# Performance work log

Hardware: AMD Instinct MI355X
Metric: run time of the kernel (lower is better)

The kernel has to match this reference:

```python
import jax, jax.numpy as jnp
import numpy as np

RCUT, RCUT_SMTH = 6.0, 0.5
NEURON = [25, 50, 100]
ATTN, NLAYER, AXIS, TEBD, NTYPES = 128, 2, 16, 8, 4
NF, NLOC, NNEI = 1, 4096, 120
LN_EPS = 1e-5


def setup_inputs() -> dict:
    key = jax.random.key(0)
    ks = jax.random.split(key, 24)
    rij = jax.random.normal(ks[0], (NF, NLOC, NNEI, 3), jnp.float32) * 2.0
    nmask = jax.random.uniform(ks[1], (NF, NLOC, NNEI)) < 0.9
    atype = jax.random.randint(ks[2], (NF, NLOC), 0, NTYPES, dtype=jnp.int32)
    ntype = jax.random.randint(ks[3], (NF, NLOC, NNEI), 0, NTYPES, dtype=jnp.int32)
    tebd = jax.random.normal(ks[4], (NTYPES, TEBD), jnp.float32) * 0.1
    dims = [1 + 2 * TEBD] + NEURON
    s = 0.1
    M = NEURON[-1]
    inp = dict(rij=rij, nmask=nmask, atype=atype, ntype=ntype, tebd=tebd)
    for i in range(3):
        inp[f'emb_w{i}'] = jax.random.normal(ks[5 + i], (dims[i], dims[i + 1]), jnp.float32) * s
        inp[f'emb_b{i}'] = jax.random.normal(ks[8 + i], (dims[i + 1],), jnp.float32) * s
    inp['wq'] = jax.random.normal(ks[11], (NLAYER, M, ATTN), jnp.float32) * s
    inp['bq'] = jax.random.normal(ks[12], (NLAYER, ATTN), jnp.float32) * s
    inp['wk'] = jax.random.normal(ks[13], (NLAYER, M, ATTN), jnp.float32) * s
    inp['bk'] = jax.random.normal(ks[14], (NLAYER, ATTN), jnp.float32) * s
    inp['wv'] = jax.random.normal(ks[15], (NLAYER, M, ATTN), jnp.float32) * s
    inp['bv'] = jax.random.normal(ks[16], (NLAYER, ATTN), jnp.float32) * s
    inp['wo'] = jax.random.normal(ks[17], (NLAYER, ATTN, M), jnp.float32) * s
    inp['bo'] = jax.random.normal(ks[18], (NLAYER, M), jnp.float32) * s
    inp['ln_g'] = jnp.ones((NLAYER, M), jnp.float32)
    inp['ln_b'] = jnp.zeros((NLAYER, M), jnp.float32)
    return inp


def _l2norm(t):
    return t / jnp.maximum(jnp.linalg.norm(t, axis=-1, keepdims=True), 1e-12)


def reference(rij, nmask, atype, ntype, tebd, emb_w0, emb_b0, emb_w1, emb_b1,
              emb_w2, emb_b2, wq, bq, wk, bk, wv, bv, wo, bo, ln_g, ln_b):
    f32 = jnp.float32
    m = nmask.astype(f32)                       # [F,N,K]
    r = jnp.linalg.norm(rij, axis=-1)           # neighbor distances
    # smooth switch function: 1 for r<rcut_smth, poly taper to 0 at rcut
    uu = jnp.clip((r - RCUT_SMTH) / (RCUT - RCUT_SMTH), 0.0, 1.0)
    sw = uu ** 3 * (-6.0 * uu ** 2 + 15.0 * uu - 10.0) + 1.0
    sr = sw / r * m                              # s(r), masked
    rhat = rij / r[..., None]                    # normalized rel. coords
    env = jnp.concatenate([sr[..., None], sr[..., None] * rhat], axis=-1)  # R^i [F,N,K,4]
    # embedding net input: s(r) ++ neighbor tebd ++ center tebd  (concat, two-side)
    t_nei = tebd[ntype]                                        # [F,N,K,TEBD]
    t_cen = jnp.broadcast_to(tebd[atype][:, :, None, :], t_nei.shape)
    x = jnp.concatenate([sr[..., None], t_nei, t_cen], axis=-1)
    h = jnp.tanh(x @ emb_w0 + emb_b0)
    h = jnp.tanh(h @ emb_w1 + emb_b1) + jnp.concatenate([h, h], -1)  # resnet (out=2*in)
    g = jnp.tanh(h @ emb_w2 + emb_b2) + jnp.concatenate([h, h], -1)  # G [F,N,K,M]
    g = g * m[..., None]
    # angular gate R_hat R_hat^T and pairwise mask / smooth weights
    gate = jnp.einsum('fnqc,fnkc->fnqk', rhat, rhat)
    sw_m = sw * m
    amask = nmask[..., :, None] & nmask[..., None, :]
    temp = float(np.sqrt(ATTN * 1.0))            # (attn*scaling_factor)**0.5
    neg = jnp.finfo(f32).min
    for l in range(NLAYER):
        q = _l2norm(g @ wq[l] + bq[l])
        k = _l2norm(g @ wk[l] + bk[l])
        v = _l2norm(g @ wv[l] + bv[l])
        scores = jnp.einsum('fnqd,fnkd->fnqk', q, k) / temp
        attnw = jax.nn.softmax(jnp.where(amask, scores, neg), axis=-1)
        attnw = attnw * amask.astype(f32)
        attnw = attnw * sw_m[..., :, None] * sw_m[..., None, :]   # smooth
        attnw = attnw * gate                                      # attn_dotr
        o = jnp.einsum('fnqk,fnkd->fnqd', attnw, v) @ wo[l] + bo[l]
        mu = o.mean(-1, keepdims=True)
        var = o.var(-1, keepdims=True)
        o = (o - mu) * jax.lax.rsqrt(var + LN_EPS) * ln_g[l] + ln_b[l]
        g = g + o                                # residual LayerNorm update
    g = g * m[..., None]
    gr = jnp.einsum('fnkc,fnkm->fncm', env, g) / NNEI            # [F,N,4,M]
    d = jnp.einsum('fncm,fnca->fnma', gr, gr[..., :AXIS])        # [F,N,M,AXIS]
    d = d.reshape(d.shape[0], d.shape[1], -1)
    return jnp.concatenate([d, tebd[atype]], axis=-1)            # concat_output_tebd
```

## Files before the change

### kernel.cpp

```cpp
#include <hip/hip_runtime.h>


#define NNEI 120
#define MDIM 100
#define ADIM 128
#define BP   136
#define H2P  72
#define XP   40
#define OUTD 1608

typedef __attribute__((ext_vector_type(8))) short bf16x8;
typedef __attribute__((ext_vector_type(4))) float f32x4;

__device__ __forceinline__ float bf2f(unsigned short u){
    return __uint_as_float(((unsigned int)u) << 16);
}
__device__ __forceinline__ unsigned short f2bf(float f){
    unsigned int x = __float_as_uint(f);
    return (unsigned short)((x + 0x7fffu + ((x >> 16) & 1u)) >> 16);
}
__device__ __forceinline__ unsigned int cvtpk(float lo, float hi){
    unsigned int r;
    asm("v_cvt_pk_bf16_f32 %0, %1, %2" : "=v"(r) : "v"(lo), "v"(hi));
    return r;
}
__device__ __forceinline__ float ftanh(float x){
    return 1.0f - 2.0f / (__expf(2.0f * x) + 1.0f);
}
__device__ __forceinline__ float red16(float v){
    v += __shfl_xor(v, 1, 64); v += __shfl_xor(v, 2, 64);
    v += __shfl_xor(v, 4, 64); v += __shfl_xor(v, 8, 64);
    return v;
}

__global__ void detect_mask_kernel(const unsigned char* __restrict__ p,
                                   int* __restrict__ flag){
    if (blockIdx.x == 0 && threadIdx.x == 0){
        const unsigned int* u = (const unsigned int*)p;
        int alli = 1, allf = 1;
        for (int i = 0; i < 64; ++i){
            unsigned int w = u[i];
            if (!(w == 0u || w == 1u)) alli = 0;
            if (!(w == 0u || w == 0x3f800000u)) allf = 0;
        }
        flag[0] = alli ? 1 : (allf ? 2 : 0);
    }
}

__global__ void prep_weights(const float* __restrict__ wq, const float* __restrict__ wk,
                             const float* __restrict__ wv, const float* __restrict__ wo,
                             const float* __restrict__ ew2, const float* __restrict__ ew0,
                             const float* __restrict__ ew1,
                             unsigned short* __restrict__ wsb){
    const int fid = blockIdx.x;
    const int lane = threadIdx.x;
    unsigned short* dst = wsb + (size_t)fid * 512 + lane * 8;
    if (fid < 192){
        const int l = fid / 96, rem = fid % 96, mat = rem / 32;
        const int r2 = rem % 32, nt = r2 / 4, ks = r2 % 4;
        const float* W = (mat == 0 ? wq : mat == 1 ? wk : wv) + l * MDIM * ADIM;
        const int nn = nt * 16 + (lane & 15);
        const int k0 = ks * 32 + (lane >> 4) * 8;
        #pragma unroll
        for (int i = 0; i < 8; ++i){
            const int kk = k0 + i;
            dst[i] = (kk < MDIM) ? f2bf(W[kk * ADIM + nn]) : (unsigned short)0;
        }
    } else if (fid < 256){
        const int f2 = fid - 192, l = f2 / 32, rem = f2 % 32, jt = rem / 4, ks = rem % 4;
        const float* W = wo + l * ADIM * MDIM;
        const int j = jt * 16 + (lane & 15);
        const int d0 = ks * 32 + (lane >> 4) * 8;
        #pragma unroll
        for (int i = 0; i < 8; ++i)
            dst[i] = (j < MDIM) ? f2bf(W[(d0 + i) * MDIM + j]) : (unsigned short)0;
    } else if (fid < 270){
        const int f3 = fid - 256, nt = f3 >> 1, ks = f3 & 1;
        const int nn = nt * 16 + (lane & 15);
        const int k0 = ks * 32 + (lane >> 4) * 8;
        #pragma unroll
        for (int i = 0; i < 8; ++i){
            const int kk = k0 + i;
            dst[i] = (kk < 50 && nn < MDIM) ? f2bf(ew2[kk * MDIM + nn]) : (unsigned short)0;
        }
    } else if (fid < 272){
        const int nt = fid - 270;
        const int nn = nt * 16 + (lane & 15);
        const int k0 = (lane >> 4) * 8;
        #pragma unroll
        for (int i = 0; i < 8; ++i){
            const int kk = k0 + i;
            dst[i] = (kk < 17 && nn < 25) ? f2bf(ew0[kk * 25 + nn]) : (unsigned short)0;
        }
    } else {
        const int nt = fid - 272;
        const int nn = nt * 16 + (lane & 15);
        const int k0 = (lane >> 4) * 8;
        #pragma unroll
        for (int i = 0; i < 8; ++i){
            const int kk = k0 + i;
            dst[i] = (kk < 25 && nn < 50) ? f2bf(ew1[kk * 50 + nn]) : (unsigned short)0;
        }
    }
}

__global__ __launch_bounds__(1024) void dpa1_kernel(
    const float* __restrict__ rij, const void* __restrict__ nmask,
    const int* __restrict__ atype, const int* __restrict__ ntype,
    const float* __restrict__ tebd,
    const float* __restrict__ eb0, const float* __restrict__ eb1,
    const float* __restrict__ eb2,
    const float* __restrict__ bq, const float* __restrict__ bk,
    const float* __restrict__ bv, const float* __restrict__ bo,
    const float* __restrict__ lng, const float* __restrict__ lnb,
    float* __restrict__ out, const int* __restrict__ flagp,
    const unsigned short* __restrict__ wsb)
{
    __shared__ __align__(16) unsigned short g16[128 * BP];
    __shared__ __align__(16) unsigned short buf1[128 * BP];
    __shared__ __align__(16) unsigned short kn_s[128 * BP];
    __shared__ __align__(16) unsigned short vT_s[128 * BP];
    __shared__ float psum_s[256];
    __shared__ float lnp_s[512];
    __shared__ __align__(16) float env_s[128 * 4];
    __shared__ __align__(16) float rhat_s[128 * 4];
    __shared__ __align__(16) float swm_s[128];
    __shared__ __align__(16) float msk_s[128];
    __shared__ float tebd_s[32];
    __shared__ float gr_s[4 * MDIM];
    __shared__ int ta_sh;

    const int n    = blockIdx.x;
    const int tid  = threadIdx.x;
    const int lane = tid & 63;
    const int wid  = tid >> 6;
    const int flag = flagp[0];
    const int l15  = lane & 15;
    const int lg4  = lane >> 4;

    if (tid < 32) tebd_s[tid] = tebd[tid];
    if (tid == 0) ta_sh = atype[n];

    {
        unsigned int* z0 = (unsigned int*)g16;
        for (int i = tid; i < 128 * (BP/2); i += 1024) z0[i] = 0;
    }
    if (tid < 128){
        const int k = tid;
        unsigned short xr[2 * XP];
        #pragma unroll
        for (int i = 0; i < 2 * XP; ++i) xr[i] = 0;
        if (k < NNEI){
            const int base = n * NNEI + k;
            const float rx = rij[base * 3 + 0];
            const float ry = rij[base * 3 + 1];
            const float rz = rij[base * 3 + 2];
            const float r  = sqrtf(rx * rx + ry * ry + rz * rz);
            float mval;
            if (flag == 1)      mval = (((const int*)nmask)[base] != 0) ? 1.0f : 0.0f;
            else if (flag == 2) mval = ((const float*)nmask)[base];
            else                mval = (((const unsigned char*)nmask)[base] != 0) ? 1.0f : 0.0f;
            float uu = (r - 0.5f) * (1.0f / 5.5f);
            uu = fminf(fmaxf(uu, 0.0f), 1.0f);
            const float sw   = uu * uu * uu * (-6.0f * uu * uu + 15.0f * uu - 10.0f) + 1.0f;
            const float invr = 1.0f / r;
            const float sr   = sw * invr * mval;
            const float hx = rx * invr, hy = ry * invr, hz = rz * invr;
            env_s[k * 4 + 0] = sr;
            env_s[k * 4 + 1] = sr * hx;
            env_s[k * 4 + 2] = sr * hy;
            env_s[k * 4 + 3] = sr * hz;
            rhat_s[k * 4 + 0] = hx; rhat_s[k * 4 + 1] = hy; rhat_s[k * 4 + 2] = hz;
            rhat_s[k * 4 + 3] = 0.0f;
            swm_s[k] = sw * mval;
            msk_s[k] = mval;
            const int tn = ntype[base] * 8;
            const int tc = atype[n] * 8;
            xr[0] = f2bf(sr);
            #pragma unroll
            for (int i = 0; i < 8; ++i){
                xr[1 + i] = f2bf(tebd[tn + i]);
                xr[9 + i] = f2bf(tebd[tc + i]);
            }
        } else {
            env_s[k*4+0] = env_s[k*4+1] = env_s[k*4+2] = env_s[k*4+3] = 0.0f;
            rhat_s[k*4+0] = rhat_s[k*4+1] = rhat_s[k*4+2] = rhat_s[k*4+3] = 0.0f;
            swm_s[k] = 0.0f; msk_s[k] = 0.0f;
        }
        #pragma unroll
        for (int c = 0; c < 5; ++c)
            *(uint4*)&kn_s[k * XP + c * 8] = *(const uint4*)&xr[c * 8];
    }
    __syncthreads();

    {
        const int mt = wid >> 1, nt = wid & 1;
        bf16x8 a = *(const bf16x8*)&kn_s[(mt*16 + l15) * XP + lg4 * 8];
        bf16x8 b = *(const bf16x8*)(wsb + (size_t)(270 + nt) * 512 + lane * 8);
        f32x4 C = (f32x4){0.f, 0.f, 0.f, 0.f};
        C = __builtin_amdgcn_mfma_f32_16x16x32_bf16(a, b, C, 0, 0, 0);
        const int j = nt * 16 + l15;
        const float ebj = (j < 25) ? eb0[j] : 0.0f;
        #pragma unroll
        for (int r = 0; r < 4; ++r){
            const int row = mt * 16 + lg4 * 4 + r;
            const float v = (row < NNEI && j < 25) ? ftanh(C[r] + ebj) : 0.0f;
            vT_s[row * XP + j] = f2bf(v);
        }
    }
    __syncthreads();

    {
        for (int jb = wid; jb < 32; jb += 16){
            const int mt = jb >> 2, nt = jb & 3;
            bf16x8 a = *(const bf16x8*)&vT_s[(mt*16 + l15) * XP + lg4 * 8];
            bf16x8 b = *(const bf16x8*)(wsb + (size_t)(272 + nt) * 512 + lane * 8);
            f32x4 C = (f32x4){0.f, 0.f, 0.f, 0.f};
            C = __builtin_amdgcn_mfma_f32_16x16x32_bf16(a, b, C, 0, 0, 0);
            const int j2 = nt * 16 + l15;
            const float ebj = (j2 < 50) ? eb1[j2] : 0.0f;
            const int jr = (j2 >= 25) ? j2 - 25 : j2;
            #pragma unroll
            for (int r = 0; r < 4; ++r){
                const int row = mt * 16 + lg4 * 4 + r;
                float v = 0.0f;
                if (row < NNEI && j2 < 50){
                    const float h1d = bf2f(vT_s[row * XP + jr]);
                    v = ftanh(C[r] + ebj) + h1d;
                }
                buf1[row * H2P + j2] = f2bf(v);
            }
        }
    }
    __syncthreads();

    {
        for (int job = wid; job < 56; job += 16){
            const int mt = job / 7, nt = job - mt * 7;
            bf16x8 a0 = *(const bf16x8*)&buf1[(mt*16 + l15) * H2P + 0*32 + lg4 * 8];
            bf16x8 a1 = *(const bf16x8*)&buf1[(mt*16 + l15) * H2P + 1*32 + lg4 * 8];
            bf16x8 b0 = *(const bf16x8*)(wsb + (size_t)(256 + nt*2 + 0) * 512 + lane * 8);
            bf16x8 b1 = *(const bf16x8*)(wsb + (size_t)(256 + nt*2 + 1) * 512 + lane * 8);
            f32x4 C = (f32x4){0.f, 0.f, 0.f, 0.f};
            C = __builtin_amdgcn_mfma_f32_16x16x32_bf16(a0, b0, C, 0, 0, 0);
            C = __builtin_amdgcn_mfma_f32_16x16x32_bf16(a1, b1, C, 0, 0, 0);
            const int j = nt * 16 + l15;
            if (j < MDIM){
                const float ebj = eb2[j];
                const int jr = (j >= 50) ? j - 50 : j;
                #pragma unroll
                for (int r = 0; r < 4; ++r){
                    const int row = mt * 16 + lg4 * 4 + r;
                    if (row < NNEI){
                        const float h2d = bf2f(buf1[row * H2P + jr]);
                        const float t = ftanh(C[r] + ebj) + h2d;
                        g16[row * BP + j] = f2bf(t * msk_s[row]);
                    }
                }
            }
        }
    }
    __syncthreads();

    const float tinv = 0.08838834764831845f;
    const int qt = wid >> 1;
    const int hh = wid & 1;
    const int q  = qt * 16 + l15;

    for (int l = 0; l < 2; ++l){
        if (wid < 8){
            bf16x8 ag[4];
            #pragma unroll
            for (int ks = 0; ks < 4; ++ks)
                ag[ks] = *(const bf16x8*)&g16[(wid*16 + l15) * BP + ks*32 + lg4 * 8];
            float qv[8][4];
            float sq[4] = {0.f, 0.f, 0.f, 0.f};
            #pragma unroll
            for (int nt = 0; nt < 8; ++nt){
                f32x4 C = (f32x4){0.f, 0.f, 0.f, 0.f};
                #pragma unroll
                for (int ks = 0; ks < 4; ++ks){
                    bf16x8 b = *(const bf16x8*)(wsb + (size_t)(((l*3+0)*8+nt)*4+ks) * 512 + lane * 8);
                    C = __builtin_amdgcn_mfma_f32_16x16x32_bf16(ag[ks], b, C, 0, 0, 0);
                }
                const float bias = bq[l * ADIM + nt*16 + l15];
                #pragma unroll
                for (int r = 0; r < 4; ++r){
                    qv[nt][r] = C[r] + bias;
                    sq[r] = fmaf(qv[nt][r], qv[nt][r], sq[r]);
                }
            }
            float qs[4];
            #pragma unroll
            for (int r = 0; r < 4; ++r)
                qs[r] = rsqrtf(fmaxf(red16(sq[r]), 1e-24f));
            #pragma unroll
            for (int nt = 0; nt < 8; ++nt)
                #pragma unroll
                for (int r = 0; r < 4; ++r)
                    buf1[(wid*16 + lg4*4 + r) * BP + nt*16 + l15] = f2bf(qv[nt][r] * qs[r]);
        } else {
            const int t = wid - 8;
            bf16x8 ag[4];
            #pragma unroll
            for (int ks = 0; ks < 4; ++ks)
                ag[ks] = *(const bf16x8*)&g16[(t*16 + l15) * BP + ks*32 + lg4 * 8];
            {
                float kv[8][4];
                float sq[4] = {0.f, 0.f, 0.f, 0.f};
                #pragma unroll
                for (int nt = 0; nt < 8; ++nt){
                    f32x4 C = (f32x4){0.f, 0.f, 0.f, 0.f};
                    #pragma unroll
                    for (int ks = 0; ks < 4; ++ks){
                        bf16x8 b = *(const bf16x8*)(wsb + (size_t)(((l*3+1)*8+nt)*4+ks) * 512 + lane * 8);
                        C = __builtin_amdgcn_mfma_f32_16x16x32_bf16(ag[ks], b, C, 0, 0, 0);
                    }
                    const float bias = bk[l * ADIM + nt*16 + l15];
                    #pragma unroll
                    for (int r = 0; r < 4; ++r){
                        kv[nt][r] = C[r] + bias;
                        sq[r] = fmaf(kv[nt][r], kv[nt][r], sq[r]);
                    }
                }
                float kss[4];
                #pragma unroll
                for (int r = 0; r < 4; ++r)
                    kss[r] = tinv * rsqrtf(fmaxf(red16(sq[r]), 1e-24f));
                #pragma unroll
                for (int nt = 0; nt < 8; ++nt)
                    #pragma unroll
                    for (int r = 0; r < 4; ++r)
                        kn_s[(t*16 + lg4*4 + r) * BP + nt*16 + l15] = f2bf(kv[nt][r] * kss[r]);
            }
            {
                float vv[8][4];
                float sq[4] = {0.f, 0.f, 0.f, 0.f};
                #pragma unroll
                for (int nt = 0; nt < 8; ++nt){
                    f32x4 C = (f32x4){0.f, 0.f, 0.f, 0.f};
                    #pragma unroll
                    for (int ks = 0; ks < 4; ++ks){
                        bf16x8 b = *(const bf16x8*)(wsb + (size_t)(((l*3+2)*8+nt)*4+ks) * 512 + lane * 8);
                        C = __builtin_amdgcn_mfma_f32_16x16x32_bf16(ag[ks], b, C, 0, 0, 0);
                    }
                    const float bias = bv[l * ADIM + nt*16 + l15];
                    #pragma unroll
                    for (int r = 0; r < 4; ++r){
                        vv[nt][r] = C[r] + bias;
                        sq[r] = fmaf(vv[nt][r], vv[nt][r], sq[r]);
                    }
                }
                float vs[4];
                #pragma unroll
                for (int r = 0; r < 4; ++r){
                    const int k = t*16 + lg4*4 + r;
                    vs[r] = swm_s[k] * rsqrtf(fmaxf(red16(sq[r]), 1e-24f));
                }
                #pragma unroll
                for (int nt = 0; nt < 8; ++nt){
                    const unsigned int lo = cvtpk(vv[nt][0]*vs[0], vv[nt][1]*vs[1]);
                    const unsigned int hi = cvtpk(vv[nt][2]*vs[2], vv[nt][3]*vs[3]);
                    *(uint2*)&vT_s[(nt*16 + l15) * BP + t*16 + lg4*4] = make_uint2(lo, hi);
                }
            }
        }
        __syncthreads();

        unsigned int pw0[4], pw1[4];
        float tot;
        {
            bf16x8 bqf[4];
            #pragma unroll
            for (int ks = 0; ks < 4; ++ks)
                bqf[ks] = *(const bf16x8*)&buf1[(qt*16 + l15) * BP + ks*32 + lg4 * 8];
            f32x4 Cs[4];
            #pragma unroll
            for (int t = 0; t < 4; ++t) Cs[t] = (f32x4){0.f, 0.f, 0.f, 0.f};
            #pragma unroll
            for (int t = 0; t < 4; ++t)
                #pragma unroll
                for (int ks = 0; ks < 4; ++ks){
                    bf16x8 a = *(const bf16x8*)&kn_s[((hh*4+t)*16 + l15) * BP + ks*32 + lg4 * 8];
                    Cs[t] = __builtin_amdgcn_mfma_f32_16x16x32_bf16(a, bqf[ks], Cs[t], 0, 0, 0);
                }
            const float4 rq = *(const float4*)&rhat_s[q * 4];
            tot = 0.f;
            #pragma unroll
            for (int t = 0; t < 4; ++t){
                const int kb = (hh*4+t)*16 + lg4*4;
                float p[4];
                #pragma unroll
                for (int r = 0; r < 4; ++r){
                    const float e = __expf(Cs[t][r]) * msk_s[kb + r];
                    tot += e;
                    const float4 rk = *(const float4*)&rhat_s[(kb + r) * 4];
                    p[r] = e * (rq.x*rk.x + rq.y*rk.y + rq.z*rk.z);
                }
                pw0[t] = cvtpk(p[0], p[1]);
                pw1[t] = cvtpk(p[2], p[3]);
            }
            tot += __shfl_xor(tot, 16, 64);
            tot += __shfl_xor(tot, 32, 64);
        }
        __syncthreads();

        #pragma unroll
        for (int t = 0; t < 4; ++t)
            *(uint2*)&buf1[(qt*16 + l15) * BP + (hh*4+t)*16 + lg4*4] = make_uint2(pw0[t], pw1[t]);
        if (lg4 == 0) psum_s[q * 2 + hh] = tot;
        __syncthreads();

        {
            bf16x8 bpf[4];
            #pragma unroll
            for (int ks = 0; ks < 4; ++ks)
                bpf[ks] = *(const bf16x8*)&buf1[(qt*16 + l15) * BP + ks*32 + lg4 * 8];
            f32x4 Co[4];
            #pragma unroll
            for (int t = 0; t < 4; ++t) Co[t] = (f32x4){0.f, 0.f, 0.f, 0.f};
            #pragma unroll
            for (int t = 0; t < 4; ++t)
                #pragma unroll
                for (int ks = 0; ks < 4; ++ks){
                    bf16x8 a = *(const bf16x8*)&vT_s[((hh*4+t)*16 + l15) * BP + ks*32 + lg4 * 8];
                    Co[t] = __builtin_amdgcn_mfma_f32_16x16x32_bf16(a, bpf[ks], Co[t], 0, 0, 0);
                }
            const float totq = psum_s[q * 2] + psum_s[q * 2 + 1];
            const float rsum = (totq > 0.0f) ? swm_s[q] / totq : 0.0f;
            #pragma unroll
            for (int t = 0; t < 4; ++t){
                const unsigned int lo = cvtpk(Co[t][0] * rsum, Co[t][1] * rsum);
                const unsigned int hi = cvtpk(Co[t][2] * rsum, Co[t][3] * rsum);
                *(uint2*)&kn_s[(qt*16 + l15) * BP + (hh*4+t)*16 + lg4*4] = make_uint2(lo, hi);
            }
        }
        __syncthreads();

        float val[4][4];
        {
            bf16x8 bof[4];
            #pragma unroll
            for (int ks = 0; ks < 4; ++ks)
                bof[ks] = *(const bf16x8*)&kn_s[(qt*16 + l15) * BP + ks*32 + lg4 * 8];
            const float* BO = bo + l * MDIM;
            float sv = 0.f, sv2 = 0.f;
            #pragma unroll
            for (int t = 0; t < 4; ++t){
                const int jt = hh*4 + t;
                f32x4 Cf = (f32x4){0.f, 0.f, 0.f, 0.f};
                #pragma unroll
                for (int ks = 0; ks < 4; ++ks){
                    bf16x8 a = *(const bf16x8*)(wsb + (size_t)(192 + (l*8+jt)*4 + ks) * 512 + lane * 8);
                    Cf = __builtin_amdgcn_mfma_f32_16x16x32_bf16(a, bof[ks], Cf, 0, 0, 0);
                }
                const bool jok = (jt < 6) || (jt == 6 && lg4 == 0);
                float4 BO4 = jok ? *(const float4*)&BO[jt*16 + lg4*4] : make_float4(0,0,0,0);
                #pragma unroll
                for (int r = 0; r < 4; ++r){
                    const float v = Cf[r] + ((const float*)&BO4)[r];
                    val[t][r] = v;
                    if (jok){ sv += v; sv2 += v * v; }
                }
            }
            sv  += __shfl_xor(sv, 16, 64);  sv  += __shfl_xor(sv, 32, 64);
            sv2 += __shfl_xor(sv2, 16, 64); sv2 += __shfl_xor(sv2, 32, 64);
            if (lg4 == 0){
                lnp_s[q * 4 + hh * 2 + 0] = sv;
                lnp_s[q * 4 + hh * 2 + 1] = sv2;
            }
        }
        __syncthreads();

        {
            const float* LG = lng + l * MDIM;
            const float* LB = lnb + l * MDIM;
            const float svt  = lnp_s[q * 4 + 0] + lnp_s[q * 4 + 2];
            const float sv2t = lnp_s[q * 4 + 1] + lnp_s[q * 4 + 3];
            const float mu   = svt * 0.01f;
            const float var  = sv2t * 0.01f - mu * mu;
            const float rstd = rsqrtf(var + 1e-5f);
            if (q < NNEI){
                #pragma unroll
                for (int t = 0; t < 4; ++t){
                    const int jt = hh*4 + t;
                    const bool jok = (jt < 6) || (jt == 6 && lg4 == 0);
                    if (jok){
                        const int jb = jt*16 + lg4*4;
                        const float4 LG4 = *(const float4*)&LG[jb];
                        const float4 LB4 = *(const float4*)&LB[jb];
                        uint2 old = *(const uint2*)&g16[q * BP + jb];
                        float nv[4];
                        nv[0] = bf2f((unsigned short)(old.x & 0xffffu))  + (val[t][0] - mu) * rstd * LG4.x + LB4.x;
                        nv[1] = bf2f((unsigned short)(old.x >> 16))      + (val[t][1] - mu) * rstd * LG4.y + LB4.y;
                        nv[2] = bf2f((unsigned short)(old.y & 0xffffu))  + (val[t][2] - mu) * rstd * LG4.z + LB4.z;
                        nv[3] = bf2f((unsigned short)(old.y >> 16))      + (val[t][3] - mu) * rstd * LG4.w + LB4.w;
                        uint2 nw;
                        nw.x = cvtpk(nv[0], nv[1]);
                        nw.y = cvtpk(nv[2], nv[3]);
                        *(uint2*)&g16[q * BP + jb] = nw;
                    }
                }
            }
        }
        __syncthreads();
    }

    for (int idx = tid; idx < 4 * MDIM; idx += 1024){
        const int c = idx / MDIM, mm = idx - c * MDIM;
        float a = 0.0f;
        for (int k = 0; k < NNEI; ++k)
            a = fmaf(env_s[k * 4 + c], bf2f(g16[k * BP + mm]), a);
        gr_s[c * MDIM + mm] = a * (1.0f / 120.0f);
    }
    __syncthreads();

    float* outp = out + (size_t)n * OUTD;
    for (int idx = tid; idx < MDIM * 16; idx += 1024){
        const int mm = idx >> 4, aa = idx & 15;
        float acc = 0.0f;
        #pragma unroll
        for (int c = 0; c < 4; ++c)
            acc = fmaf(gr_s[c * MDIM + mm], gr_s[c * MDIM + aa], acc);
        outp[idx] = acc;
    }
    if (tid < 8) outp[1600 + tid] = tebd_s[ta_sh * 8 + tid];
}

extern "C" void kernel_launch(void* const* d_in, const int* in_sizes, int n_in,
                              void* d_out, int out_size, void* d_ws, size_t ws_size,
                              hipStream_t stream) {
    const float* rij   = (const float*)d_in[0];
    const void*  nmask = d_in[1];
    const int*   atype = (const int*)d_in[2];
    const int*   ntype = (const int*)d_in[3];
    const float* tebd  = (const float*)d_in[4];
    const float* ew0 = (const float*)d_in[5];
    const float* eb0 = (const float*)d_in[6];
    const float* ew1 = (const float*)d_in[7];
    const float* eb1 = (const float*)d_in[8];
    const float* ew2 = (const float*)d_in[9];
    const float* eb2 = (const float*)d_in[10];
    const float* wq = (const float*)d_in[11];
    const float* bq = (const float*)d_in[12];
    const float* wk = (const float*)d_in[13];
    const float* bk = (const float*)d_in[14];
    const float* wv = (const float*)d_in[15];
    const float* bv = (const float*)d_in[16];
    const float* wo = (const float*)d_in[17];
    const float* bo = (const float*)d_in[18];
    const float* lng = (const float*)d_in[19];
    const float* lnb = (const float*)d_in[20];
    float* out = (float*)d_out;
    int* flag = (int*)d_ws;
    unsigned short* wsb = (unsigned short*)((char*)d_ws + 256);

    detect_mask_kernel<<<1, 64, 0, stream>>>((const unsigned char*)nmask, flag);
    prep_weights<<<276, 64, 0, stream>>>(wq, wk, wv, wo, ew2, ew0, ew1, wsb);
    dpa1_kernel<<<4096, 1024, 0, stream>>>(rij, nmask, atype, ntype, tebd,
                                           eb0, eb1, eb2,
                                           bq, bk, bv, bo, lng, lnb,
                                           out, flag, wsb);
}
```

Measured before the change: 744.4 us.

## Balance Q/K/V projection work across all 16 waves with deferred Q normalization

Previously waves 0-7 computed Q while waves 8-15 computed both K and V, so the load was uneven. Now waves 0-7 compute K, waves 8-15 compute V, and every wave computes half of the Q columns. Q is stored unnormalized, its squared norms are accumulated into shared memory with atomics, and the normalization is applied as a scale on the scores before exp. This shortens the critical path of the projection phase, at the cost of LDS atomics, an extra reset of the norm buffer, and a small bf16 rounding difference because Q is rounded before it is normalized.

```diff
diff --git a/kernel.cpp b/kernel.cpp
--- a/kernel.cpp
+++ b/kernel.cpp
@@ -122,6 +122,7 @@
     __shared__ __align__(16) unsigned short vT_s[128 * BP];
     __shared__ float psum_s[256];
     __shared__ float lnp_s[512];
+    __shared__ float qss_s[128];
     __shared__ __align__(16) float env_s[128 * 4];
     __shared__ __align__(16) float rhat_s[128 * 4];
     __shared__ __align__(16) float swm_s[128];
@@ -259,6 +260,7 @@
                 }
             }
         }
+        if (tid < 128) qss_s[tid] = 0.0f;
     }
     __syncthreads();
 
@@ -268,44 +270,13 @@
     const int q  = qt * 16 + l15;
 
     for (int l = 0; l < 2; ++l){
-        if (wid < 8){
-            bf16x8 ag[4];
-            #pragma unroll
-            for (int ks = 0; ks < 4; ++ks)
-                ag[ks] = *(const bf16x8*)&g16[(wid*16 + l15) * BP + ks*32 + lg4 * 8];
-            float qv[8][4];
-            float sq[4] = {0.f, 0.f, 0.f, 0.f};
-            #pragma unroll
-            for (int nt = 0; nt < 8; ++nt){
-                f32x4 C = (f32x4){0.f, 0.f, 0.f, 0.f};
-                #pragma unroll
-                for (int ks = 0; ks < 4; ++ks){
-                    bf16x8 b = *(const bf16x8*)(wsb + (size_t)(((l*3+0)*8+nt)*4+ks) * 512 + lane * 8);
-                    C = __builtin_amdgcn_mfma_f32_16x16x32_bf16(ag[ks], b, C, 0, 0, 0);
-                }
-                const float bias = bq[l * ADIM + nt*16 + l15];
-                #pragma unroll
-                for (int r = 0; r < 4; ++r){
-                    qv[nt][r] = C[r] + bias;
-                    sq[r] = fmaf(qv[nt][r], qv[nt][r], sq[r]);
-                }
-            }
-            float qs[4];
-            #pragma unroll
-            for (int r = 0; r < 4; ++r)
-                qs[r] = rsqrtf(fmaxf(red16(sq[r]), 1e-24f));
-            #pragma unroll
-            for (int nt = 0; nt < 8; ++nt)
-                #pragma unroll
-                for (int r = 0; r < 4; ++r)
-                    buf1[(wid*16 + lg4*4 + r) * BP + nt*16 + l15] = f2bf(qv[nt][r] * qs[r]);
-        } else {
-            const int t = wid - 8;
+        {
+            const int t = wid & 7;
             bf16x8 ag[4];
             #pragma unroll
             for (int ks = 0; ks < 4; ++ks)
                 ag[ks] = *(const bf16x8*)&g16[(t*16 + l15) * BP + ks*32 + lg4 * 8];
-            {
+            if (wid < 8){
                 float kv[8][4];
                 float sq[4] = {0.f, 0.f, 0.f, 0.f};
                 #pragma unroll
@@ -332,8 +303,7 @@
                     #pragma unroll
                     for (int r = 0; r < 4; ++r)
                         kn_s[(t*16 + lg4*4 + r) * BP + nt*16 + l15] = f2bf(kv[nt][r] * kss[r]);
-            }
-            {
+            } else {
                 float vv[8][4];
                 float sq[4] = {0.f, 0.f, 0.f, 0.f};
                 #pragma unroll
@@ -364,6 +334,35 @@
                     *(uint2*)&vT_s[(nt*16 + l15) * BP + t*16 + lg4*4] = make_uint2(lo, hi);
                 }
             }
+            {
+                bf16x8 aq[4];
+                #pragma unroll
+                for (int ks = 0; ks < 4; ++ks)
+                    aq[ks] = *(const bf16x8*)&g16[(qt*16 + l15) * BP + ks*32 + lg4 * 8];
+                float sq2[4] = {0.f, 0.f, 0.f, 0.f};
+                #pragma unroll
+                for (int u = 0; u < 4; ++u){
+                    const int nt = hh*4 + u;
+                    f32x4 C = (f32x4){0.f, 0.f, 0.f, 0.f};
+                    #pragma unroll
+                    for (int ks = 0; ks < 4; ++ks){
+                        bf16x8 b = *(const bf16x8*)(wsb + (size_t)(((l*3+0)*8+nt)*4+ks) * 512 + lane * 8);
+                        C = __builtin_amdgcn_mfma_f32_16x16x32_bf16(aq[ks], b, C, 0, 0, 0);
+                    }
+                    const float bias = bq[l * ADIM + nt*16 + l15];
+                    #pragma unroll
+                    for (int r = 0; r < 4; ++r){
+                        const float v = C[r] + bias;
+                        buf1[(qt*16 + lg4*4 + r) * BP + nt*16 + l15] = f2bf(v);
+                        sq2[r] = fmaf(v, v, sq2[r]);
+                    }
+                }
+                #pragma unroll
+                for (int r = 0; r < 4; ++r){
+                    const float s = red16(sq2[r]);
+                    if (l15 == 0) atomicAdd(&qss_s[qt*16 + lg4*4 + r], s);
+                }
+            }
         }
         __syncthreads();
 
@@ -384,6 +383,7 @@
                     bf16x8 a = *(const bf16x8*)&kn_s[((hh*4+t)*16 + l15) * BP + ks*32 + lg4 * 8];
                     Cs[t] = __builtin_amdgcn_mfma_f32_16x16x32_bf16(a, bqf[ks], Cs[t], 0, 0, 0);
                 }
+            const float qi = rsqrtf(fmaxf(qss_s[q], 1e-24f));
             const float4 rq = *(const float4*)&rhat_s[q * 4];
             tot = 0.f;
             #pragma unroll
@@ -392,7 +392,7 @@
                 float p[4];
                 #pragma unroll
                 for (int r = 0; r < 4; ++r){
-                    const float e = __expf(Cs[t][r]) * msk_s[kb + r];
+                    const float e = __expf(Cs[t][r] * qi) * msk_s[kb + r];
                     tot += e;
                     const float4 rk = *(const float4*)&rhat_s[(kb + r) * 4];
                     p[r] = e * (rq.x*rk.x + rq.y*rk.y + rq.z*rk.z);
@@ -502,6 +502,7 @@
                     }
                 }
             }
+            if (tid < 128) qss_s[tid] = 0.0f;
         }
         __syncthreads();
     }
```

After: 746.0 us. About the same (+0.2%).
